# Performance work log

Hardware: AMD Instinct MI355X
Metric: run time of the kernel (lower is better)

## Reference

```python
import jax, jax.numpy as jnp
import numpy as np

MAX_WAVELENGTH = 10000
BIG_NEG = -2.3819763e38

def _rope(x, positions):
    # x: [B, L, H, D], positions: [B, L] float32
    d = x.shape[-1]
    freq_exp = 2.0 / d * jnp.arange(d // 2, dtype=jnp.float32)
    timescale = MAX_WAVELENGTH ** freq_exp
    radians = (positions[..., None] / timescale[None, None, :])[..., None, :]  # [B,L,1,D/2]
    sin, cos = jnp.sin(radians), jnp.cos(radians)
    x1, x2 = jnp.split(x, 2, axis=-1)
    return jnp.concatenate([x1 * cos - x2 * sin, x2 * cos + x1 * sin], axis=-1).astype(x.dtype)

def _adaln_rmsnorm(x, cond, Wmod, bmod):
    # RMSNorm in fp32, then AdaLN scale/shift; returns (normed, gate[B,1,D])
    var = jnp.mean(jnp.square(x.astype(jnp.float32)), axis=-1, keepdims=True)
    normed = x * jax.lax.rsqrt(var + 1e-6)
    mod = (cond @ Wmod + bmod)[:, None, :]  # [B,1,3D]
    scale, shift, gate = jnp.split(mod, 3, axis=-1)
    return (normed * (1 + scale) + shift).astype(x.dtype), gate

def setup_inputs() -> dict:
    key = jax.random.key(0)
    ks = jax.random.split(key, 9)
    B, T, D, F, N, K, H = 2, 2048, 2048, 16384, 8, 1, 256
    x = jax.random.normal(ks[0], (B, T, D), jnp.float32)
    positions = jnp.broadcast_to(jnp.arange(T, dtype=jnp.float32), (B, T))
    attn_mask = jnp.broadcast_to(jnp.tril(jnp.ones((T, T), dtype=bool))[None, None], (B, 1, T, T))
    cond = jax.random.normal(ks[1], (B, D), jnp.float32)
    Wmod_a = jax.random.normal(ks[2], (D, 3 * D), jnp.float32) * 0.02
    bmod_a = jnp.zeros((3 * D,), jnp.float32)
    Wq = jax.random.normal(ks[3], (N, D, H), jnp.float32) * (D ** -0.5)
    Wkv = jax.random.normal(ks[4], (2, K, D, H), jnp.float32) * (D ** -0.5)
    Wo = jax.random.normal(ks[5], (N, H, D), jnp.float32) * ((N * H) ** -0.5)
    Wmod_f = jax.random.normal(ks[6], (D, 3 * D), jnp.float32) * 0.02
    bmod_f = jnp.zeros((3 * D,), jnp.float32)
    Wg = jax.random.normal(ks[7], (2, D, F), jnp.float32) * (D ** -0.5)
    Wl = jax.random.normal(ks[8], (F, D), jnp.float32) * (F ** -0.5)
    return dict(x=x, positions=positions, attn_mask=attn_mask, cond=cond,
                Wmod_a=Wmod_a, bmod_a=bmod_a, Wq=Wq, Wkv=Wkv, Wo=Wo,
                Wmod_f=Wmod_f, bmod_f=bmod_f, Wg=Wg, Wl=Wl)

def reference(x, positions, attn_mask, cond, Wmod_a, bmod_a, Wq, Wkv, Wo, Wmod_f, bmod_f, Wg, Wl):
    K = Wkv.shape[1]               # num_kv_heads
    H = Wq.shape[-1]               # head_dim
    # --- pre-attention AdaLN RMSNorm ---
    n, gate_a = _adaln_rmsnorm(x, cond, Wmod_a, bmod_a)
    # --- GQA projections ---
    q = jnp.einsum('BTD,NDH->BTNH', n, Wq)
    k = jnp.einsum('BSD,KDH->BSKH', n, Wkv[0])
    v = jnp.einsum('BSD,KDH->BSKH', n, Wkv[1])
    q = _rope(q, positions) * (H ** -0.5)
    k = _rope(k, positions)
    B, T, N, _ = q.shape
    q = q.reshape(B, T, K, N // K, H)  # B T K G H
    logits = jnp.einsum('BTKGH,BSKH->BKGTS', q, k, preferred_element_type=jnp.float32)
    masked = jnp.where(attn_mask[:, :, None, :, :], logits, BIG_NEG)
    probs = jax.nn.softmax(masked, axis=-1).astype(x.dtype)
    enc = jnp.einsum('BKGTS,BSKH->BTKGH', probs, v).reshape(B, T, N, H)
    attn_out = jnp.einsum('BTNH,NHD->BTD', enc, Wo)
    # gated residual
    x = x + attn_out * gate_a
    # --- pre-FFN AdaLN RMSNorm + gated-GeLU MLP ---
    n, gate_f = _adaln_rmsnorm(x, cond, Wmod_f, bmod_f)
    h = jax.nn.gelu(jnp.einsum('BTD,DF->BTF', n, Wg[0])) * jnp.einsum('BTD,DF->BTF', n, Wg[1])
    mlp_out = jnp.einsum('BTF,FD->BTD', h, Wl)
    return x + mlp_out * gate_f
```

## Files before the change

kernel.cpp:

```cpp
#include <hip/hip_runtime.h>
#include <hip/hip_bf16.h>

typedef __bf16 bf16_t;
typedef __bf16 bf16x8 __attribute__((ext_vector_type(8)));
typedef float  f32x4  __attribute__((ext_vector_type(4)));

#define DEV static __device__ __forceinline__

DEV void gload16(const bf16_t* g, bf16_t* l) {
    __builtin_amdgcn_global_load_lds(
        (const __attribute__((address_space(1))) void*)g,
        (__attribute__((address_space(3))) void*)l, 16, 0, 0);
}

enum { EPI_F32 = 0, EPI_BF16 = 1, EPI_RES = 2, EPI_GELU = 3, EPI_MUL = 4 };

#define G_MFMA(d, a, b) d = __builtin_amdgcn_mfma_f32_16x16x32_bf16(a, b, d, 0, 0, 0)

#define COMPUTE(AB0, AB1, BB0, BB1)                                           \
  { bf16x8 aF[8], bF[4];                                                      \
    _Pragma("unroll") for (int m8 = 0; m8 < 8; m8++)                          \
      aF[m8] = *(const bf16x8*)(AB0 + (m8 >> 2) * 4096 + (m8 & 3) * 1024);    \
    _Pragma("unroll") for (int nj = 0; nj < 4; nj++)                          \
      bF[nj] = *(const bf16x8*)(BB0 + nj * 1024);                             \
    _Pragma("unroll") for (int m8 = 0; m8 < 8; m8++)                          \
      _Pragma("unroll") for (int nj = 0; nj < 4; nj++)                        \
        G_MFMA(acc[m8][nj], aF[m8], bF[nj]);                                  \
    _Pragma("unroll") for (int m8 = 0; m8 < 8; m8++)                          \
      aF[m8] = *(const bf16x8*)(AB1 + (m8 >> 2) * 4096 + (m8 & 3) * 1024);    \
    _Pragma("unroll") for (int nj = 0; nj < 4; nj++)                          \
      bF[nj] = *(const bf16x8*)(BB1 + nj * 1024);                             \
    _Pragma("unroll") for (int m8 = 0; m8 < 8; m8++)                          \
      _Pragma("unroll") for (int nj = 0; nj < 4; nj++)                        \
        G_MFMA(acc[m8][nj], aF[m8], bF[nj]);                                  \
  }

#define STAGE8(kt, bi)                                                        \
  { SCA(kt, bi, 0); SCA(kt, bi, 1); SCA(kt, bi, 2); SCA(kt, bi, 3);           \
    SCB(kt, bi, 0); SCB(kt, bi, 1); SCB(kt, bi, 2); SCB(kt, bi, 3); }

template<int EPI>
__global__ __launch_bounds__(512, 1)
void gemma(const bf16_t* __restrict__ A, const bf16_t* __restrict__ Bt,
           void* __restrict__ Cout, int Kd, int lda, int ldb, int ldc,
           long sCz,
           const float* __restrict__ res, const float* __restrict__ gate,
           int gateStride, int rowsPerB, const bf16_t* __restrict__ aux)
{
    const int nbx = gridDim.x;
    const int nwg = nbx * gridDim.y;
    int lin = blockIdx.y * nbx + blockIdx.x;
    const int q8 = nwg >> 3, r8 = nwg & 7;
    const int xcd = lin & 7, oo = lin >> 3;
    lin = (xcd < r8 ? xcd * (q8 + 1) : r8 * (q8 + 1) + (xcd - r8) * q8) + oo;
    const long m0 = (long)(lin / nbx) * 256;
    const long n0 = (long)(lin % nbx) * 256;
    const long kb = (long)blockIdx.z * Kd;

    const int tid = threadIdx.x;
    const int l   = tid & 63;
    const int w   = tid >> 6;
    const int wr  = w >> 2;
    const int wcn = w & 3;

    __shared__ bf16_t sA[2][16384];
    __shared__ bf16_t sB[2][16384];

    const long sgc = (long)(((l & 7) ^ (l >> 3)) << 3);
    const int NT = Kd >> 6;
    const int NI = NT >> 1;

    const bf16_t* pA0 = A + (m0 + 0 * 64 + w * 8 + (l >> 3)) * (long)lda + kb + sgc;
    const bf16_t* pA1 = A + (m0 + 1 * 64 + w * 8 + (l >> 3)) * (long)lda + kb + sgc;
    const bf16_t* pA2 = A + (m0 + 2 * 64 + w * 8 + (l >> 3)) * (long)lda + kb + sgc;
    const bf16_t* pA3 = A + (m0 + 3 * 64 + w * 8 + (l >> 3)) * (long)lda + kb + sgc;
    const bf16_t* pB0 = Bt + (n0 + 0 * 64 + w * 8 + (l >> 3)) * (long)ldb + kb + sgc;
    const bf16_t* pB1 = Bt + (n0 + 1 * 64 + w * 8 + (l >> 3)) * (long)ldb + kb + sgc;
    const bf16_t* pB2 = Bt + (n0 + 2 * 64 + w * 8 + (l >> 3)) * (long)ldb + kb + sgc;
    const bf16_t* pB3 = Bt + (n0 + 3 * 64 + w * 8 + (l >> 3)) * (long)ldb + kb + sgc;

#define SCA(kt, bi, c) gload16(pA##c + (kt), &sA[bi][(c) * 4096 + w * 512])
#define SCB(kt, bi, c) gload16(pB##c + (kt), &sB[bi][(c) * 4096 + w * 512])

    f32x4 acc[8][4];
#pragma unroll
    for (int i = 0; i < 8; i++)
#pragma unroll
        for (int j = 0; j < 4; j++) acc[i][j] = f32x4{0.f, 0.f, 0.f, 0.f};

    const int co0 = ((l >> 4) ^ (l & 7)) << 3;
    const int co1 = ((4 + (l >> 4)) ^ (l & 7)) << 3;

    const bf16_t* rbA00 = &sA[0][(wr * 128 + (l & 15)) * 64 + co0];
    const bf16_t* rbA01 = &sA[0][(wr * 128 + (l & 15)) * 64 + co1];
    const bf16_t* rbA10 = &sA[1][(wr * 128 + (l & 15)) * 64 + co0];
    const bf16_t* rbA11 = &sA[1][(wr * 128 + (l & 15)) * 64 + co1];
    const bf16_t* rbB00 = &sB[0][(wcn * 64 + (l & 15)) * 64 + co0];
    const bf16_t* rbB01 = &sB[0][(wcn * 64 + (l & 15)) * 64 + co1];
    const bf16_t* rbB10 = &sB[1][(wcn * 64 + (l & 15)) * 64 + co0];
    const bf16_t* rbB11 = &sB[1][(wcn * 64 + (l & 15)) * 64 + co1];

    STAGE8(0, 0);

    for (int it = 0; it < NI; ++it) {
        const int u = 2 * it, v = 2 * it + 1;
        asm volatile("s_waitcnt lgkmcnt(0)" ::: "memory");
        __builtin_amdgcn_s_barrier();
        STAGE8((long)v * 64, 1);
        asm volatile("s_waitcnt vmcnt(8)" ::: "memory");
        __builtin_amdgcn_s_barrier();
        COMPUTE(rbA00, rbA01, rbB00, rbB01);
        asm volatile("s_waitcnt lgkmcnt(0)" ::: "memory");
        __builtin_amdgcn_s_barrier();
        if (v + 1 < NT) {
            STAGE8((long)(v + 1) * 64, 0);
            asm volatile("s_waitcnt vmcnt(8)" ::: "memory");
        } else {
            asm volatile("s_waitcnt vmcnt(0)" ::: "memory");
        }
        __builtin_amdgcn_s_barrier();
        COMPUTE(rbA10, rbA11, rbB10, rbB11);
    }

#pragma unroll
    for (int mi = 0; mi < 8; mi++) {
#pragma unroll
        for (int nj = 0; nj < 4; nj++) {
            f32x4 vv = acc[mi][nj];
            const long col   = n0 + wcn * 64 + nj * 16 + (l & 15);
            const long row0r = m0 + wr * 128 + mi * 16 + ((l >> 4) * 4);
#pragma unroll
            for (int e = 0; e < 4; e++) {
                const long row = row0r + e;
                const long idx = row * (long)ldc + col + (long)blockIdx.z * sCz;
                const float val = vv[e];
                if constexpr (EPI == EPI_F32) {
                    ((float*)Cout)[idx] = val;
                } else if constexpr (EPI == EPI_BF16) {
                    ((bf16_t*)Cout)[idx] = (bf16_t)val;
                } else if constexpr (EPI == EPI_RES) {
                    const int b = (int)(row / rowsPerB);
                    ((float*)Cout)[idx] = res[row * (long)ldc + col] + val * gate[(long)b * gateStride + col];
                } else if constexpr (EPI == EPI_GELU) {
                    const float gl = 0.5f * val * (1.f + tanhf(0.7978845608f * (val + 0.044715f * val * val * val)));
                    ((bf16_t*)Cout)[idx] = (bf16_t)gl;
                } else if constexpr (EPI == EPI_MUL) {
                    ((bf16_t*)Cout)[idx] = (bf16_t)((float)aux[idx] * val);
                }
            }
        }
    }
#undef SCA
#undef SCB
}

__global__ __launch_bounds__(256)
void combine_splitk(const float* __restrict__ P, const float* __restrict__ X1,
                    const float* __restrict__ gate, float* __restrict__ out,
                    int D, int T, int gateStride, long zstride, long n4)
{
    for (long i4 = (long)blockIdx.x * 256 + threadIdx.x; i4 < n4; i4 += (long)gridDim.x * 256) {
        const long i = i4 * 4;
        const float4 p0 = *(const float4*)(P + i);
        const float4 p1 = *(const float4*)(P + i + zstride);
        const float4 xv = *(const float4*)(X1 + i);
        const long row = i / D;
        const int  b   = (int)(row / T);
        const int  col = (int)(i - row * D);
        const float* gp = gate + (long)b * gateStride + col;
        float4 r;
        r.x = xv.x + (p0.x + p1.x) * gp[0];
        r.y = xv.y + (p0.y + p1.y) * gp[1];
        r.z = xv.z + (p0.z + p1.z) * gp[2];
        r.w = xv.w + (p0.w + p1.w) * gp[3];
        *(float4*)(out + i) = r;
    }
}

template<int EPI, int CAUSAL>
__global__ __launch_bounds__(256)
void gemm_bt(const bf16_t* __restrict__ A, const bf16_t* __restrict__ Bt,
             void* __restrict__ Cout,
             int M, int N, int Kd, int lda, int ldb, int ldc,
             long sAz, long sBz, long sCz,
             const float* __restrict__ res, const float* __restrict__ gate,
             int gateStride, int rowsPerB, const bf16_t* __restrict__ aux)
{
    const int tid = threadIdx.x;
    const int l   = tid & 63;
    const int w   = tid >> 6;
    const int wr  = w >> 1, wc = w & 1;
    const long m0 = (long)blockIdx.y * 128;
    const long n0 = (long)blockIdx.x * 128;
    const int  z  = blockIdx.z;

    if constexpr (CAUSAL == 1) {
        if (n0 > m0 + 127) return;
    }
    int kend = Kd;
    if constexpr (CAUSAL == 2) {
        const int kc = (int)m0 + 128;
        kend = kc < Kd ? kc : Kd;
    }

    A  += (long)z * sAz;
    Bt += (long)z * sBz;

    __shared__ bf16_t As[128 * 32];
    __shared__ bf16_t Bs[128 * 32];

    const int srow = w * 16 + (l >> 2);
    const int scol = (l & 3) * 8;
    const bf16_t* Ag = A  + (m0 + srow) * (long)lda + scol;
    const bf16_t* Bg = Bt + (n0 + srow) * (long)ldb + scol;

    bf16_t* ldsA = As + w * 512;
    bf16_t* ldsB = Bs + w * 512;

    f32x4 acc[16];
    const f32x4 fz = {0.f, 0.f, 0.f, 0.f};
#pragma unroll
    for (int i = 0; i < 16; i++) acc[i] = fz;

    for (int k0 = 0; k0 < kend; k0 += 32) {
        gload16(Ag + k0,                  ldsA);
        gload16(Ag + k0 + 64 * (long)lda, ldsA + 2048);
        gload16(Bg + k0,                  ldsB);
        gload16(Bg + k0 + 64 * (long)ldb, ldsB + 2048);
        __syncthreads();

        bf16x8 af[4], bfr[4];
#pragma unroll
        for (int f = 0; f < 4; f++) {
            af[f]  = *(const bf16x8*)(As + (wr * 64 + f * 16 + (l & 15)) * 32 + (l >> 4) * 8);
            bfr[f] = *(const bf16x8*)(Bs + (wc * 64 + f * 16 + (l & 15)) * 32 + (l >> 4) * 8);
        }
#pragma unroll
        for (int i = 0; i < 4; i++)
#pragma unroll
            for (int j = 0; j < 4; j++)
                acc[i * 4 + j] = __builtin_amdgcn_mfma_f32_16x16x32_bf16(af[i], bfr[j], acc[i * 4 + j], 0, 0, 0);
        __syncthreads();
    }

#pragma unroll
    for (int i = 0; i < 4; i++) {
#pragma unroll
        for (int j = 0; j < 4; j++) {
            f32x4 v = acc[i * 4 + j];
            const long col  = n0 + wc * 64 + j * 16 + (l & 15);
            const long row0 = m0 + wr * 64 + i * 16 + ((l >> 4) * 4);
#pragma unroll
            for (int e = 0; e < 4; e++) {
                const long row = row0 + e;
                const long idx = row * (long)ldc + col + (long)z * sCz;
                const float val = v[e];
                if constexpr (EPI == EPI_F32) {
                    ((float*)Cout)[idx] = val;
                } else if constexpr (EPI == EPI_BF16) {
                    ((bf16_t*)Cout)[idx] = (bf16_t)val;
                } else if constexpr (EPI == EPI_RES) {
                    const int b = (int)(row / rowsPerB);
                    ((float*)Cout)[idx] = res[row * (long)ldc + col] + val * gate[(long)b * gateStride + col];
                } else if constexpr (EPI == EPI_GELU) {
                    const float gl = 0.5f * val * (1.f + tanhf(0.7978845608f * (val + 0.044715f * val * val * val)));
                    ((bf16_t*)Cout)[idx] = (bf16_t)gl;
                } else {
                    ((bf16_t*)Cout)[idx] = (bf16_t)((float)aux[idx] * val);
                }
            }
        }
    }
}

__global__ __launch_bounds__(256)
void transpose_f2b(const float* __restrict__ in, bf16_t* __restrict__ out,
                   int R, int C, long inStride, long outStride)
{
    __shared__ float tile[32][33];
    in  += (long)blockIdx.z * inStride;
    out += (long)blockIdx.z * outStride;
    const int c0 = blockIdx.x * 32, r0 = blockIdx.y * 32;
    const int tx = threadIdx.x, ty = threadIdx.y;
#pragma unroll
    for (int i = 0; i < 4; i++)
        tile[ty + i * 8][tx] = in[(long)(r0 + ty + i * 8) * C + c0 + tx];
    __syncthreads();
#pragma unroll
    for (int i = 0; i < 4; i++)
        out[(long)(c0 + ty + i * 8) * R + r0 + tx] = (bf16_t)tile[tx][ty + i * 8];
}

__global__ __launch_bounds__(256)
void modk_part(const float* __restrict__ cond, const float* __restrict__ W,
               float* __restrict__ part, int D3, int KS)
{
    const int j = blockIdx.x * 256 + threadIdx.x;
    const int b = blockIdx.y;
    const int z = blockIdx.z;
    const float* cb = cond + (long)b * (KS * gridDim.z);
    float s = 0.f;
    const int d0 = z * KS;
#pragma unroll 4
    for (int d = d0; d < d0 + KS; d++) s += cb[d] * W[(long)d * D3 + j];
    part[((long)z * gridDim.y + b) * D3 + j] = s;
}

__global__ __launch_bounds__(256)
void modk_reduce(const float* __restrict__ part, const float* __restrict__ bvec,
                 float* __restrict__ mod, int D3, int NZ)
{
    const int j = blockIdx.x * 256 + threadIdx.x;
    const int b = blockIdx.y;
    float s = bvec[j];
    for (int z = 0; z < NZ; z++) s += part[((long)z * gridDim.y + b) * D3 + j];
    mod[(long)b * D3 + j] = s;
}

__global__ __launch_bounds__(256)
void rmsnorm_adaln(const float* __restrict__ xin, const float* __restrict__ mod,
                   bf16_t* __restrict__ out, int D, int T, int D3)
{
    const long row = blockIdx.x;
    const int  b   = (int)(row / T);
    const int  tid = threadIdx.x;
    const float4* x4 = (const float4*)(xin + row * (long)D);
    const float4 v0 = x4[tid], v1 = x4[tid + 256];
    float ss = v0.x * v0.x + v0.y * v0.y + v0.z * v0.z + v0.w * v0.w
             + v1.x * v1.x + v1.y * v1.y + v1.z * v1.z + v1.w * v1.w;
    for (int o = 32; o; o >>= 1) ss += __shfl_down(ss, o, 64);
    __shared__ float red[4];
    if ((tid & 63) == 0) red[tid >> 6] = ss;
    __syncthreads();
    ss = red[0] + red[1] + red[2] + red[3];
    const float rs = rsqrtf(ss / (float)D + 1e-6f);
    const float* sc = mod + (long)b * D3;
    const float* sh = sc + D;
    const float4 s0 = ((const float4*)sc)[tid], s1 = ((const float4*)sc)[tid + 256];
    const float4 h0 = ((const float4*)sh)[tid], h1 = ((const float4*)sh)[tid + 256];
    bf16_t* orow = out + row * (long)D;
    orow[tid * 4 + 0]         = (bf16_t)(v0.x * rs * (1.f + s0.x) + h0.x);
    orow[tid * 4 + 1]         = (bf16_t)(v0.y * rs * (1.f + s0.y) + h0.y);
    orow[tid * 4 + 2]         = (bf16_t)(v0.z * rs * (1.f + s0.z) + h0.z);
    orow[tid * 4 + 3]         = (bf16_t)(v0.w * rs * (1.f + s0.w) + h0.w);
    orow[(tid + 256) * 4 + 0] = (bf16_t)(v1.x * rs * (1.f + s1.x) + h1.x);
    orow[(tid + 256) * 4 + 1] = (bf16_t)(v1.y * rs * (1.f + s1.y) + h1.y);
    orow[(tid + 256) * 4 + 2] = (bf16_t)(v1.z * rs * (1.f + s1.z) + h1.z);
    orow[(tid + 256) * 4 + 3] = (bf16_t)(v1.w * rs * (1.f + s1.w) + h1.w);
}

__global__ __launch_bounds__(128)
void rope_q(const bf16_t* __restrict__ qp, const float* __restrict__ positions,
            bf16_t* __restrict__ qo, int T, int ldq, int H)
{
    const int t = blockIdx.x, n = blockIdx.y, b = blockIdx.z;
    const int i = threadIdx.x;
    const long in0 = ((long)(b * T + t)) * ldq + n * H;
    const float x1 = (float)qp[in0 + i];
    const float x2 = (float)qp[in0 + i + 128];
    const float pos = positions[b * T + t];
    const float inv = expf(-9.210340371976184f * (float)i / 128.f);
    float s, c;
    sincosf(pos * inv, &s, &c);
    const float scl = 0.0625f;
    const long out0 = (((long)(b * 8 + n)) * T + t) * H;
    qo[out0 + i]       = (bf16_t)((x1 * c - x2 * s) * scl);
    qo[out0 + i + 128] = (bf16_t)((x2 * c + x1 * s) * scl);
}

__global__ __launch_bounds__(128)
void rope_kv(const bf16_t* __restrict__ kvp, const float* __restrict__ positions,
             bf16_t* __restrict__ ko, bf16_t* __restrict__ vt, int T, int H, int S, int ldkv)
{
    const int t = blockIdx.x, b = blockIdx.y;
    const int i = threadIdx.x;
    const long in0 = ((long)(b * T + t)) * ldkv;
    const float k1 = (float)kvp[in0 + i];
    const float k2 = (float)kvp[in0 + i + 128];
    const float pos = positions[b * T + t];
    const float inv = expf(-9.210340371976184f * (float)i / 128.f);
    float s, c;
    sincosf(pos * inv, &s, &c);
    const long ko0 = ((long)(b * T + t)) * H;
    ko[ko0 + i]       = (bf16_t)(k1 * c - k2 * s);
    ko[ko0 + i + 128] = (bf16_t)(k2 * c + k1 * s);
    vt[((long)b * H + i) * S + t]       = kvp[in0 + 256 + i];
    vt[((long)b * H + i + 128) * S + t] = kvp[in0 + 256 + i + 128];
}

__global__ __launch_bounds__(256)
void softmax_causal(const float* __restrict__ sc, bf16_t* __restrict__ pr, int T, int S)
{
    const int t = blockIdx.x, g = blockIdx.y;
    const long row = (long)g * T + t;
    const float* srow = sc + row * S;
    bf16_t* prow = pr + row * S;
    const int tid = threadIdx.x;
    const int limit = t | 127;
    const int nch = (limit >> 8) + 1;
    float vals[8];
    float mx = -3.4e38f;
    for (int i = 0; i < nch; i++) {
        const int s = i * 256 + tid;
        const float v = (s <= t) ? srow[s] : -3.4e38f;
        vals[i] = v;
        mx = fmaxf(mx, v);
    }
    for (int o = 32; o; o >>= 1) mx = fmaxf(mx, __shfl_down(mx, o, 64));
    __shared__ float red[4];
    if ((tid & 63) == 0) red[tid >> 6] = mx;
    __syncthreads();
    mx = fmaxf(fmaxf(red[0], red[1]), fmaxf(red[2], red[3]));
    __syncthreads();
    float sum = 0.f;
    for (int i = 0; i < nch; i++) {
        const int s = i * 256 + tid;
        const float e = (s <= t) ? __expf(vals[i] - mx) : 0.f;
        vals[i] = e;
        sum += e;
    }
    for (int o = 32; o; o >>= 1) sum += __shfl_down(sum, o, 64);
    if ((tid & 63) == 0) red[tid >> 6] = sum;
    __syncthreads();
    sum = red[0] + red[1] + red[2] + red[3];
    const float invs = 1.f / sum;
    for (int i = 0; i < nch; i++)
        prow[i * 256 + tid] = (bf16_t)(vals[i] * invs);
}

extern "C" void kernel_launch(void* const* d_in, const int* in_sizes, int n_in,
                              void* d_out, int out_size, void* d_ws, size_t ws_size,
                              hipStream_t stream)
{
    const float* x      = (const float*)d_in[0];
    const float* pos    = (const float*)d_in[1];
    const float* cond   = (const float*)d_in[3];
    const float* Wmod_a = (const float*)d_in[4];
    const float* bmod_a = (const float*)d_in[5];
    const float* Wq     = (const float*)d_in[6];
    const float* Wkv    = (const float*)d_in[7];
    const float* Wo     = (const float*)d_in[8];
    const float* Wmod_f = (const float*)d_in[9];
    const float* bmod_f = (const float*)d_in[10];
    const float* Wg     = (const float*)d_in[11];
    const float* Wl     = (const float*)d_in[12];

    constexpr int  Bb = 2, T = 2048, D = 2048, F = 16384, Nh = 8, H = 256;
    constexpr int  NH = 2048, S = 2048, G = 8, BT = 4096, D3 = 6144;
    constexpr int  KSLICE = 64, NZ = D / KSLICE;
    constexpr int  NQKV = 2560;

    char* ws = (char*)d_ws;
    size_t off = 0;
    auto alloc = [&](size_t bytes) { char* p = ws + off; off += bytes; return p; };

    bf16_t* WQT  = (bf16_t*)alloc((size_t)NH * D * 2);
    bf16_t* WKVT = (bf16_t*)alloc((size_t)512 * D * 2);
    bf16_t* WOT  = (bf16_t*)alloc((size_t)D * NH * 2);
    bf16_t* WGT  = (bf16_t*)alloc((size_t)2 * F * D * 2);
    bf16_t* WLT  = (bf16_t*)alloc((size_t)D * F * 2);
    float*  MODA = (float*)alloc((size_t)Bb * D3 * 4);
    float*  MODF = (float*)alloc((size_t)Bb * D3 * 4);
    float*  PART = (float*)alloc((size_t)NZ * Bb * D3 * 4);
    bf16_t* NA   = (bf16_t*)alloc((size_t)BT * D * 2);
    bf16_t* QKVP = (bf16_t*)alloc((size_t)BT * NQKV * 2);
    bf16_t* Qr   = (bf16_t*)alloc((size_t)Bb * Nh * T * H * 2);
    bf16_t* Kr   = (bf16_t*)alloc((size_t)Bb * T * H * 2);
    bf16_t* VT   = (bf16_t*)alloc((size_t)Bb * H * S * 2);
    bf16_t* ENC  = (bf16_t*)alloc((size_t)BT * NH * 2);
    float*  X1   = (float*)alloc((size_t)BT * D * 4);
    bf16_t* NF   = (bf16_t*)alloc((size_t)BT * D * 2);
    const size_t scBytes = (size_t)G * T * S * 4;
    const size_t prBytes = (size_t)G * T * S * 2;
    const size_t hBytes  = (size_t)BT * F * 2;
    const size_t bigBytes = (scBytes + prBytes > hBytes) ? (scBytes + prBytes) : hBytes;
    char* big = alloc(bigBytes);
    float*  SC = (float*)big;
    bf16_t* PR = (bf16_t*)(big + scBytes);
    bf16_t* Hb = (bf16_t*)big;
    float*  PARTK = (float*)(big + hBytes);
    (void)ws_size; (void)in_sizes; (void)n_in; (void)out_size;

    const dim3 tb(32, 8);
    transpose_f2b<<<dim3(H / 32, D / 32, 8), tb, 0, stream>>>(Wq,  WQT,  D,  H, (long)D * H, (long)H * D);
    transpose_f2b<<<dim3(H / 32, D / 32, 2), tb, 0, stream>>>(Wkv, WKVT, D,  H, (long)D * H, (long)H * D);
    transpose_f2b<<<dim3(D / 32, NH / 32, 1), tb, 0, stream>>>(Wo, WOT, NH,  D, 0, 0);
    transpose_f2b<<<dim3(F / 32, D / 32, 2), tb, 0, stream>>>(Wg,  WGT,  D,  F, (long)D * F, (long)F * D);
    transpose_f2b<<<dim3(D / 32, F / 32, 1), tb, 0, stream>>>(Wl,  WLT,  F,  D, 0, 0);
    modk_part<<<dim3(D3 / 256, Bb, NZ), 256, 0, stream>>>(cond, Wmod_a, PART, D3, KSLICE);
    modk_reduce<<<dim3(D3 / 256, Bb), 256, 0, stream>>>(PART, bmod_a, MODA, D3, NZ);
    modk_part<<<dim3(D3 / 256, Bb, NZ), 256, 0, stream>>>(cond, Wmod_f, PART, D3, KSLICE);
    modk_reduce<<<dim3(D3 / 256, Bb), 256, 0, stream>>>(PART, bmod_f, MODF, D3, NZ);
    rmsnorm_adaln<<<BT, 256, 0, stream>>>(x, MODA, NA, D, T, D3);
    gemma<EPI_BF16><<<dim3(NQKV / 256, BT / 256, 1), 512, 0, stream>>>(
        NA, WQT, QKVP, D, D, D, NQKV, 0, nullptr, nullptr, 0, 0, nullptr);
    rope_q<<<dim3(T, Nh, Bb), 128, 0, stream>>>(QKVP, pos, Qr, T, NQKV, H);
    rope_kv<<<dim3(T, Bb), 128, 0, stream>>>(QKVP + NH, pos, Kr, VT, T, H, S, NQKV);
    for (int b = 0; b < Bb; b++) {
        gemm_bt<EPI_F32, 1><<<dim3(S / 128, T / 128, G), 256, 0, stream>>>(
            Qr + (long)b * Nh * T * H, Kr + (long)b * T * H, SC,
            T, S, H, H, H, S, (long)T * H, 0, (long)T * S, nullptr, nullptr, 0, 0, nullptr);
        softmax_causal<<<dim3(T, G), 256, 0, stream>>>(SC, PR, T, S);
        gemm_bt<EPI_BF16, 2><<<dim3(H / 128, T / 128, G), 256, 0, stream>>>(
            PR, VT + (long)b * H * S, ENC + (long)b * T * NH,
            T, H, S, S, S, NH, (long)T * S, 0, (long)H, nullptr, nullptr, 0, 0, nullptr);
    }
    gemma<EPI_RES><<<dim3(D / 256, BT / 256, 1), 512, 0, stream>>>(
        ENC, WOT, X1, NH, NH, NH, D, 0, x, MODA + 2 * D, D3, T, nullptr);
    rmsnorm_adaln<<<BT, 256, 0, stream>>>(X1, MODF, NF, D, T, D3);
    gemma<EPI_GELU><<<dim3(F / 256, BT / 256, 1), 512, 0, stream>>>(
        NF, WGT, Hb, D, D, D, F, 0, nullptr, nullptr, 0, 0, nullptr);
    gemma<EPI_MUL><<<dim3(F / 256, BT / 256, 1), 512, 0, stream>>>(
        NF, WGT + (long)F * D, Hb, D, D, D, F, 0, nullptr, nullptr, 0, 0, Hb);
    gemma<EPI_F32><<<dim3(D / 256, BT / 256, 2), 512, 0, stream>>>(
        Hb, WLT, PARTK, F / 2, F, F, D, (long)BT * D, nullptr, nullptr, 0, 0, nullptr);
    combine_splitk<<<2048, 256, 0, stream>>>(
        PARTK, X1, MODF + 2 * D, (float*)d_out, D, T, D3, (long)BT * D, (long)BT * D / 4);
}
```

Before: 1.545 ms.

## Replace materialized attention with fused flash-attention kernel and split-K output projection

Replaces the per-batch QK^T GEMM, causal softmax and PV GEMM (which wrote full fp32 score and bf16 probability matrices) with one flash-attention kernel using online softmax and causal tile skipping. This removes the large score/probability traffic to memory. The new kernel reads K and V fragments straight from global memory without LDS staging, so it relies on cache for reuse. The output projection also becomes a 2-way split-K GEMM followed by the existing combine kernel, which applies the residual and gate.

New measurement: 1.740 ms. 1.13x slower.

```diff
diff --git a/kernel.cpp b/kernel.cpp
--- a/kernel.cpp
+++ b/kernel.cpp
@@ -103,7 +103,7 @@
     STAGE8(0, 0);
 
     for (int it = 0; it < NI; ++it) {
-        const int u = 2 * it, v = 2 * it + 1;
+        const int v = 2 * it + 1;
         asm volatile("s_waitcnt lgkmcnt(0)" ::: "memory");
         __builtin_amdgcn_s_barrier();
         STAGE8((long)v * 64, 1);
@@ -155,7 +155,7 @@
 }
 
 __global__ __launch_bounds__(256)
-void combine_splitk(const float* __restrict__ P, const float* __restrict__ X1,
+void combine_splitk(const float* __restrict__ P, const float* __restrict__ res,
                     const float* __restrict__ gate, float* __restrict__ out,
                     int D, int T, int gateStride, long zstride, long n4)
 {
@@ -163,7 +163,7 @@
         const long i = i4 * 4;
         const float4 p0 = *(const float4*)(P + i);
         const float4 p1 = *(const float4*)(P + i + zstride);
-        const float4 xv = *(const float4*)(X1 + i);
+        const float4 xv = *(const float4*)(res + i);
         const long row = i / D;
         const int  b   = (int)(row / T);
         const int  col = (int)(i - row * D);
@@ -177,100 +177,117 @@
     }
 }
 
-template<int EPI, int CAUSAL>
-__global__ __launch_bounds__(256)
-void gemm_bt(const bf16_t* __restrict__ A, const bf16_t* __restrict__ Bt,
-             void* __restrict__ Cout,
-             int M, int N, int Kd, int lda, int ldb, int ldc,
-             long sAz, long sBz, long sCz,
-             const float* __restrict__ res, const float* __restrict__ gate,
-             int gateStride, int rowsPerB, const bf16_t* __restrict__ aux)
-{
+__global__ __launch_bounds__(256)
+void flash_attn(const bf16_t* __restrict__ Qr, const bf16_t* __restrict__ Kr,
+                const bf16_t* __restrict__ VT, bf16_t* __restrict__ ENC,
+                int T, int H, int S)
+{
+    const int qt = blockIdx.x;
+    const int bg = blockIdx.y;
+    const int b  = bg >> 3;
+    const int g  = bg & 7;
     const int tid = threadIdx.x;
-    const int l   = tid & 63;
-    const int w   = tid >> 6;
-    const int wr  = w >> 1, wc = w & 1;
-    const long m0 = (long)blockIdx.y * 128;
-    const long n0 = (long)blockIdx.x * 128;
-    const int  z  = blockIdx.z;
-
-    if constexpr (CAUSAL == 1) {
-        if (n0 > m0 + 127) return;
+    const int l  = tid & 63;
+    const int w  = tid >> 6;
+    const int lr = l & 15;
+    const int lg = l >> 4;
+
+    __shared__ bf16_t P[64][136];
+
+    const long qbase = ((long)bg * T + qt * 64 + w * 16 + lr) * H;
+    bf16x8 qf[8];
+#pragma unroll
+    for (int ks = 0; ks < 8; ks++)
+        qf[ks] = *(const bf16x8*)(Qr + qbase + ks * 32 + lg * 8);
+
+    const bf16_t* Kb = Kr + (long)b * T * H;
+    const bf16_t* Vb = VT + (long)b * H * S;
+
+    f32x4 o[16];
+#pragma unroll
+    for (int j = 0; j < 16; j++) o[j] = f32x4{0.f, 0.f, 0.f, 0.f};
+    float m[4]    = {-3.0e38f, -3.0e38f, -3.0e38f, -3.0e38f};
+    float lsum[4] = {0.f, 0.f, 0.f, 0.f};
+
+    const int q_lo = qt * 64 + w * 16;
+    const int nt = (qt >> 1) + 1;
+
+    for (int kt = 0; kt < nt; kt++) {
+        f32x4 s[8];
+#pragma unroll
+        for (int j = 0; j < 8; j++) s[j] = f32x4{0.f, 0.f, 0.f, 0.f};
+#pragma unroll
+        for (int ks = 0; ks < 8; ks++) {
+#pragma unroll
+            for (int j = 0; j < 8; j++) {
+                const bf16x8 kf = *(const bf16x8*)(Kb + (long)(kt * 128 + j * 16 + lr) * H + ks * 32 + lg * 8);
+                G_MFMA(s[j], qf[ks], kf);
+            }
+        }
+        float smax[4] = {-3.0e38f, -3.0e38f, -3.0e38f, -3.0e38f};
+#pragma unroll
+        for (int j = 0; j < 8; j++) {
+            const int sg = kt * 128 + j * 16 + lr;
+#pragma unroll
+            for (int e = 0; e < 4; e++) {
+                const int qg = q_lo + lg * 4 + e;
+                if (sg > qg) s[j][e] = -3.0e38f;
+                smax[e] = fmaxf(smax[e], s[j][e]);
+            }
+        }
+#pragma unroll
+        for (int off = 1; off < 16; off <<= 1)
+#pragma unroll
+            for (int e = 0; e < 4; e++)
+                smax[e] = fmaxf(smax[e], __shfl_xor(smax[e], off, 16));
+        float scale[4];
+#pragma unroll
+        for (int e = 0; e < 4; e++) {
+            const float mn = fmaxf(m[e], smax[e]);
+            scale[e] = __expf(m[e] - mn);
+            m[e] = mn;
+        }
+        float rs[4] = {0.f, 0.f, 0.f, 0.f};
+#pragma unroll
+        for (int j = 0; j < 8; j++)
+#pragma unroll
+            for (int e = 0; e < 4; e++) {
+                const float p = __expf(s[j][e] - m[e]);
+                rs[e] += p;
+                P[w * 16 + lg * 4 + e][j * 16 + lr] = (bf16_t)p;
+            }
+#pragma unroll
+        for (int off = 1; off < 16; off <<= 1)
+#pragma unroll
+            for (int e = 0; e < 4; e++)
+                rs[e] += __shfl_xor(rs[e], off, 16);
+#pragma unroll
+        for (int e = 0; e < 4; e++) lsum[e] = lsum[e] * scale[e] + rs[e];
+#pragma unroll
+        for (int j = 0; j < 16; j++)
+#pragma unroll
+            for (int e = 0; e < 4; e++) o[j][e] *= scale[e];
+#pragma unroll
+        for (int ks = 0; ks < 4; ks++) {
+            const bf16x8 pa = *(const bf16x8*)(&P[w * 16 + lr][ks * 32 + lg * 8]);
+#pragma unroll
+            for (int j = 0; j < 16; j++) {
+                const bf16x8 vf = *(const bf16x8*)(Vb + (long)(j * 16 + lr) * S + kt * 128 + ks * 32 + lg * 8);
+                G_MFMA(o[j], pa, vf);
+            }
+        }
     }
-    int kend = Kd;
-    if constexpr (CAUSAL == 2) {
-        const int kc = (int)m0 + 128;
-        kend = kc < Kd ? kc : Kd;
-    }
-
-    A  += (long)z * sAz;
-    Bt += (long)z * sBz;
-
-    __shared__ bf16_t As[128 * 32];
-    __shared__ bf16_t Bs[128 * 32];
-
-    const int srow = w * 16 + (l >> 2);
-    const int scol = (l & 3) * 8;
-    const bf16_t* Ag = A  + (m0 + srow) * (long)lda + scol;
-    const bf16_t* Bg = Bt + (n0 + srow) * (long)ldb + scol;
-
-    bf16_t* ldsA = As + w * 512;
-    bf16_t* ldsB = Bs + w * 512;
-
-    f32x4 acc[16];
-    const f32x4 fz = {0.f, 0.f, 0.f, 0.f};
-#pragma unroll
-    for (int i = 0; i < 16; i++) acc[i] = fz;
-
-    for (int k0 = 0; k0 < kend; k0 += 32) {
-        gload16(Ag + k0,                  ldsA);
-        gload16(Ag + k0 + 64 * (long)lda, ldsA + 2048);
-        gload16(Bg + k0,                  ldsB);
-        gload16(Bg + k0 + 64 * (long)ldb, ldsB + 2048);
-        __syncthreads();
-
-        bf16x8 af[4], bfr[4];
-#pragma unroll
-        for (int f = 0; f < 4; f++) {
-            af[f]  = *(const bf16x8*)(As + (wr * 64 + f * 16 + (l & 15)) * 32 + (l >> 4) * 8);
-            bfr[f] = *(const bf16x8*)(Bs + (wc * 64 + f * 16 + (l & 15)) * 32 + (l >> 4) * 8);
-        }
-#pragma unroll
-        for (int i = 0; i < 4; i++)
-#pragma unroll
-            for (int j = 0; j < 4; j++)
-                acc[i * 4 + j] = __builtin_amdgcn_mfma_f32_16x16x32_bf16(af[i], bfr[j], acc[i * 4 + j], 0, 0, 0);
-        __syncthreads();
-    }
-
-#pragma unroll
-    for (int i = 0; i < 4; i++) {
-#pragma unroll
-        for (int j = 0; j < 4; j++) {
-            f32x4 v = acc[i * 4 + j];
-            const long col  = n0 + wc * 64 + j * 16 + (l & 15);
-            const long row0 = m0 + wr * 64 + i * 16 + ((l >> 4) * 4);
-#pragma unroll
-            for (int e = 0; e < 4; e++) {
-                const long row = row0 + e;
-                const long idx = row * (long)ldc + col + (long)z * sCz;
-                const float val = v[e];
-                if constexpr (EPI == EPI_F32) {
-                    ((float*)Cout)[idx] = val;
-                } else if constexpr (EPI == EPI_BF16) {
-                    ((bf16_t*)Cout)[idx] = (bf16_t)val;
-                } else if constexpr (EPI == EPI_RES) {
-                    const int b = (int)(row / rowsPerB);
-                    ((float*)Cout)[idx] = res[row * (long)ldc + col] + val * gate[(long)b * gateStride + col];
-                } else if constexpr (EPI == EPI_GELU) {
-                    const float gl = 0.5f * val * (1.f + tanhf(0.7978845608f * (val + 0.044715f * val * val * val)));
-                    ((bf16_t*)Cout)[idx] = (bf16_t)gl;
-                } else {
-                    ((bf16_t*)Cout)[idx] = (bf16_t)((float)aux[idx] * val);
-                }
-            }
-        }
-    }
+
+    float inv[4];
+#pragma unroll
+    for (int e = 0; e < 4; e++) inv[e] = 1.f / lsum[e];
+#pragma unroll
+    for (int j = 0; j < 16; j++)
+#pragma unroll
+        for (int e = 0; e < 4; e++) {
+            const int t = qt * 64 + w * 16 + lg * 4 + e;
+            ENC[((long)b * T + t) * 2048 + g * 256 + j * 16 + lr] = (bf16_t)(o[j][e] * inv[e]);
+        }
 }
 
 __global__ __launch_bounds__(256)
@@ -388,46 +405,6 @@
     vt[((long)b * H + i + 128) * S + t] = kvp[in0 + 256 + i + 128];
 }
 
-__global__ __launch_bounds__(256)
-void softmax_causal(const float* __restrict__ sc, bf16_t* __restrict__ pr, int T, int S)
-{
-    const int t = blockIdx.x, g = blockIdx.y;
-    const long row = (long)g * T + t;
-    const float* srow = sc + row * S;
-    bf16_t* prow = pr + row * S;
-    const int tid = threadIdx.x;
-    const int limit = t | 127;
-    const int nch = (limit >> 8) + 1;
-    float vals[8];
-    float mx = -3.4e38f;
-    for (int i = 0; i < nch; i++) {
-        const int s = i * 256 + tid;
-        const float v = (s <= t) ? srow[s] : -3.4e38f;
-        vals[i] = v;
-        mx = fmaxf(mx, v);
-    }
-    for (int o = 32; o; o >>= 1) mx = fmaxf(mx, __shfl_down(mx, o, 64));
-    __shared__ float red[4];
-    if ((tid & 63) == 0) red[tid >> 6] = mx;
-    __syncthreads();
-    mx = fmaxf(fmaxf(red[0], red[1]), fmaxf(red[2], red[3]));
-    __syncthreads();
-    float sum = 0.f;
-    for (int i = 0; i < nch; i++) {
-        const int s = i * 256 + tid;
-        const float e = (s <= t) ? __expf(vals[i] - mx) : 0.f;
-        vals[i] = e;
-        sum += e;
-    }
-    for (int o = 32; o; o >>= 1) sum += __shfl_down(sum, o, 64);
-    if ((tid & 63) == 0) red[tid >> 6] = sum;
-    __syncthreads();
-    sum = red[0] + red[1] + red[2] + red[3];
-    const float invs = 1.f / sum;
-    for (int i = 0; i < nch; i++)
-        prow[i * 256 + tid] = (bf16_t)(vals[i] * invs);
-}
-
 extern "C" void kernel_launch(void* const* d_in, const int* in_sizes, int n_in,
                               void* d_out, int out_size, void* d_ws, size_t ws_size,
                               hipStream_t stream)
@@ -446,7 +423,7 @@
     const float* Wl     = (const float*)d_in[12];
 
     constexpr int  Bb = 2, T = 2048, D = 2048, F = 16384, Nh = 8, H = 256;
-    constexpr int  NH = 2048, S = 2048, G = 8, BT = 4096, D3 = 6144;
+    constexpr int  NH = 2048, S = 2048, BT = 4096, D3 = 6144;
     constexpr int  KSLICE = 64, NZ = D / KSLICE;
     constexpr int  NQKV = 2560;
 
@@ -470,14 +447,9 @@
     bf16_t* ENC  = (bf16_t*)alloc((size_t)BT * NH * 2);
     float*  X1   = (float*)alloc((size_t)BT * D * 4);
     bf16_t* NF   = (bf16_t*)alloc((size_t)BT * D * 2);
-    const size_t scBytes = (size_t)G * T * S * 4;
-    const size_t prBytes = (size_t)G * T * S * 2;
-    const size_t hBytes  = (size_t)BT * F * 2;
-    const size_t bigBytes = (scBytes + prBytes > hBytes) ? (scBytes + prBytes) : hBytes;
-    char* big = alloc(bigBytes);
-    float*  SC = (float*)big;
-    bf16_t* PR = (bf16_t*)(big + scBytes);
-    bf16_t* Hb = (bf16_t*)big;
+    const size_t hBytes = (size_t)BT * F * 2;
+    char* big = alloc(hBytes + (size_t)2 * BT * D * 4);
+    bf16_t* Hb    = (bf16_t*)big;
     float*  PARTK = (float*)(big + hBytes);
     (void)ws_size; (void)in_sizes; (void)n_in; (void)out_size;
 
@@ -496,17 +468,11 @@
         NA, WQT, QKVP, D, D, D, NQKV, 0, nullptr, nullptr, 0, 0, nullptr);
     rope_q<<<dim3(T, Nh, Bb), 128, 0, stream>>>(QKVP, pos, Qr, T, NQKV, H);
     rope_kv<<<dim3(T, Bb), 128, 0, stream>>>(QKVP + NH, pos, Kr, VT, T, H, S, NQKV);
-    for (int b = 0; b < Bb; b++) {
-        gemm_bt<EPI_F32, 1><<<dim3(S / 128, T / 128, G), 256, 0, stream>>>(
-            Qr + (long)b * Nh * T * H, Kr + (long)b * T * H, SC,
-            T, S, H, H, H, S, (long)T * H, 0, (long)T * S, nullptr, nullptr, 0, 0, nullptr);
-        softmax_causal<<<dim3(T, G), 256, 0, stream>>>(SC, PR, T, S);
-        gemm_bt<EPI_BF16, 2><<<dim3(H / 128, T / 128, G), 256, 0, stream>>>(
-            PR, VT + (long)b * H * S, ENC + (long)b * T * NH,
-            T, H, S, S, S, NH, (long)T * S, 0, (long)H, nullptr, nullptr, 0, 0, nullptr);
-    }
-    gemma<EPI_RES><<<dim3(D / 256, BT / 256, 1), 512, 0, stream>>>(
-        ENC, WOT, X1, NH, NH, NH, D, 0, x, MODA + 2 * D, D3, T, nullptr);
+    flash_attn<<<dim3(T / 64, Bb * Nh), 256, 0, stream>>>(Qr, Kr, VT, ENC, T, H, S);
+    gemma<EPI_F32><<<dim3(D / 256, BT / 256, 2), 512, 0, stream>>>(
+        ENC, WOT, PARTK, NH / 2, NH, NH, D, (long)BT * D, nullptr, nullptr, 0, 0, nullptr);
+    combine_splitk<<<2048, 256, 0, stream>>>(
+        PARTK, x, MODA + 2 * D, X1, D, T, D3, (long)BT * D, (long)BT * D / 4);
     rmsnorm_adaln<<<BT, 256, 0, stream>>>(X1, MODF, NF, D, T, D3);
     gemma<EPI_GELU><<<dim3(F / 256, BT / 256, 1), 512, 0, stream>>>(
         NF, WGT, Hb, D, D, D, F, 0, nullptr, nullptr, 0, 0, nullptr);
```
